# Performance work log

Hardware: AMD Instinct MI355X
Metric: run time of the kernel (lower is better)

The kernel has to match this reference:

```python
import jax, jax.numpy as jnp
import numpy as np

NUM_HEADS = 8
WS = 7          # window size (hardcoded in source)
SR = 4          # sr_ratio
EPS = 1e-5


def _win_partition(t, ws, H, W):
    # t: [B, h, N, d] -> [B*h*nW, ws*ws, d]
    B, h, N, d = t.shape
    t = t.reshape(B * h, H // ws, ws, W // ws, ws, d)
    t = t.transpose(0, 1, 3, 2, 4, 5)
    return t.reshape(-1, ws * ws, d)


def _win_reverse(w, ws, H, W, h):
    # w: [B*h*nW, ws*ws, d] -> [B, H*W, h*d]
    d = w.shape[-1]
    Bh = w.shape[0] // ((H // ws) * (W // ws))
    x = w.reshape(Bh, H // ws, W // ws, ws, ws, d).transpose(0, 1, 3, 2, 4, 5)
    x = x.reshape(Bh // h, h, H, W, d).transpose(0, 2, 3, 1, 4)
    return x.reshape(Bh // h, H * W, h * d)


def setup_inputs() -> dict:
    key = jax.random.key(0)
    B, H, W, C = 32, 56, 56, 256
    N = H * W
    ks = jax.random.split(key, 10)
    s = lambda k, shp: jax.random.normal(k, shp, dtype=jnp.float32) * 0.02
    return {
        "x": jax.random.normal(ks[0], (B, N, C), dtype=jnp.float32),
        "lepe_lin_w": s(ks[1], (C, C)), "lepe_lin_b": jnp.zeros((C,), jnp.float32),
        "lepe_conv_w": s(ks[2], (3, 3, 1, C)), "lepe_conv_b": jnp.zeros((C,), jnp.float32),
        "sr_w": s(ks[3], (SR, SR, C, C)), "sr_b": jnp.zeros((C,), jnp.float32),
        "norm_g": jnp.ones((C,), jnp.float32), "norm_b": jnp.zeros((C,), jnp.float32),
        "q1_w": s(ks[4], (C, C // 2)), "kv1_w": s(ks[5], (C, C)),
        "q2_w": s(ks[6], (C, C // 2)), "kv2_w": s(ks[7], (C, C)),
        "proj_w": s(ks[8], (C, C)), "proj_b": jnp.zeros((C,), jnp.float32),
        "H": H, "W": W,
    }


def reference(x, lepe_lin_w, lepe_lin_b, lepe_conv_w, lepe_conv_b, sr_w, sr_b,
              norm_g, norm_b, q1_w, kv1_w, q2_w, kv2_w, proj_w, proj_b, H, W):
    B, N, C = x.shape
    h2 = NUM_HEADS // 2
    d = C // NUM_HEADS
    scale = d ** (-0.5)

    # lepe: linear -> depthwise 3x3 conv (NHWC) -> flatten back
    lep = (x @ lepe_lin_w + lepe_lin_b).reshape(B, H, W, C)
    lep = jax.lax.conv_general_dilated(
        lep, lepe_conv_w, window_strides=(1, 1), padding='SAME',
        dimension_numbers=('NHWC', 'HWIO', 'NHWC'), feature_group_count=C) + lepe_conv_b
    lepe = lep.reshape(B, N, C)

    # --- branch 1: global attention over sr-downsampled kv ---
    q1 = (x @ q1_w).reshape(B, N, h2, d).transpose(0, 2, 1, 3)         # [B,h2,N,d]
    img = x.reshape(B, H, W, C)
    x1_ = jax.lax.conv_general_dilated(
        img, sr_w, window_strides=(SR, SR), padding='VALID',
        dimension_numbers=('NHWC', 'HWIO', 'NHWC')) + sr_b              # [B,H/sr,W/sr,C]
    x1_ = x1_.reshape(B, -1, C)                                         # [B,N1,C]
    mu = jnp.mean(x1_, axis=-1, keepdims=True)
    var = jnp.mean(jnp.square(x1_ - mu), axis=-1, keepdims=True)
    x1_ = (x1_ - mu) * jax.lax.rsqrt(var + EPS) * norm_g + norm_b
    x1_ = jax.nn.gelu(x1_, approximate=False)
    kv1 = (x1_ @ kv1_w).reshape(B, -1, 2, h2, d).transpose(2, 0, 3, 1, 4)
    k1, v1 = kv1[0], kv1[1]                                             # [B,h2,N1,d]
    attn1 = jax.nn.softmax(jnp.einsum('bhnd,bhmd->bhnm', q1, k1) * scale, axis=-1)
    x1 = jnp.einsum('bhnm,bhmd->bhnd', attn1, v1)
    x1 = x1.transpose(0, 2, 1, 3).reshape(B, N, C // 2)

    # --- branch 2: 7x7 window attention ---
    q2 = (x @ q2_w).reshape(B, N, h2, d).transpose(0, 2, 1, 3)          # [B,h2,N,d]
    kv2 = (x @ kv2_w).reshape(B, -1, 2, h2, d).transpose(2, 0, 3, 1, 4)
    k2, v2 = kv2[0], kv2[1]
    q2w = _win_partition(q2, WS, H, W)                                  # [B*h2*nW,49,d]
    k2w = _win_partition(k2, WS, H, W)
    v2w = _win_partition(v2, WS, H, W)
    attn2 = jax.nn.softmax(jnp.einsum('wnd,wmd->wnm', q2w, k2w) * scale, axis=-1)
    x2w = jnp.einsum('wnm,wmd->wnd', attn2, v2w)
    x2 = _win_reverse(x2w, WS, H, W, h2)                                # [B,N,C/2]

    out = jnp.concatenate([x1, x2], axis=-1)
    out = (out + lepe) @ proj_w + proj_b
    return out
```

## Files before the change

### kernel.cpp

```cpp
#include <hip/hip_runtime.h>
#include <hip/hip_bf16.h>

typedef __hip_bfloat16 bf16;
typedef __attribute__((ext_vector_type(8))) short short8;
typedef __attribute__((ext_vector_type(4))) float floatx4;

__device__ __forceinline__ float toF(bf16 v){ return __bfloat162float(v); }
__device__ __forceinline__ float b2f(unsigned short u){
  return __uint_as_float(((unsigned int)u) << 16);
}
__device__ __forceinline__ unsigned short f2bu(float f){
  bf16 h = __float2bfloat16(f);
  return *(unsigned short*)&h;
}

__device__ __forceinline__ void gl2l16(const void* g, void* l) {
  __builtin_amdgcn_global_load_lds(
      (const __attribute__((address_space(1))) unsigned int*)g,
      (__attribute__((address_space(3))) unsigned int*)l, 16, 0, 0);
}

__global__ __launch_bounds__(256) void cvt_x_kernel(
    const float* __restrict__ in, bf16* __restrict__ out) {
  size_t i4 = ((size_t)blockIdx.x * 256 + threadIdx.x) * 4;
  float4 v = *(const float4*)(in + i4);
  ushort4 o;
  o.x = f2bu(v.x); o.y = f2bu(v.y); o.z = f2bu(v.z); o.w = f2bu(v.w);
  *(ushort4*)(out + i4) = o;
}

__global__ __launch_bounds__(256) void prep_kernel(
    const float* __restrict__ sr_w, const float* __restrict__ lepe_w,
    const float* __restrict__ kv2_w, const float* __restrict__ q1_w,
    const float* __restrict__ q2_w, const float* __restrict__ kv1_w,
    const float* __restrict__ proj_w,
    bf16* __restrict__ wT_sr, bf16* __restrict__ wT_x,
    bf16* __restrict__ wT_kv1, bf16* __restrict__ wT_proj,
    int* __restrict__ srbase) {
  const int bid = blockIdx.x, tid = threadIdx.x;
  const float* src; bf16* dst; int K, N, idx;
  if (bid < 4096)      { src = sr_w;   dst = wT_sr;          K = 4096; N = 256; idx = bid * 256 + tid; }
  else if (bid < 4352) { src = lepe_w; dst = wT_x;           K = 256;  N = 256; idx = (bid - 4096) * 256 + tid; }
  else if (bid < 4608) { src = kv2_w;  dst = wT_x + 65536;   K = 256;  N = 256; idx = (bid - 4352) * 256 + tid; }
  else if (bid < 4736) { src = q1_w;   dst = wT_x + 131072;  K = 256;  N = 128; idx = (bid - 4608) * 256 + tid; }
  else if (bid < 4864) { src = q2_w;   dst = wT_x + 163840;  K = 256;  N = 128; idx = (bid - 4736) * 256 + tid; }
  else if (bid < 5120) { src = kv1_w;  dst = wT_kv1;         K = 256;  N = 256; idx = (bid - 4864) * 256 + tid; }
  else if (bid < 5376) { src = proj_w; dst = wT_proj;        K = 256;  N = 256; idx = (bid - 5120) * 256 + tid; }
  else {
    int t = (bid - 5376) * 256 + tid;
    if (t < 6272) {
      int b = t / 196, p = t - b * 196;
      int oy = p / 14, ox = p - oy * 14;
      srbase[t] = ((b * 56 + oy * 4) * 56 + ox * 4) * 256;
    }
    return;
  }
  int k = idx / N, n = idx - k * N;
  dst[(size_t)n * K + k] = __float2bfloat16(src[idx]);
}

__global__ __launch_bounds__(256) void gemm_mfma_f(
    const bf16* __restrict__ A, const bf16* __restrict__ BT,
    float* __restrict__ C, int K, int N) {
  __shared__ bf16 As[2][128 * 32];
  __shared__ bf16 Bs[2][128 * 32];
  const int tid = threadIdx.x;
  const int m0 = blockIdx.y * 128;
  const int n0 = blockIdx.x * 128;
  const int wave = tid >> 6, lane = tid & 63;
  const int wm = (wave >> 1) * 64, wn = (wave & 1) * 64;
  const int l15 = lane & 15, quad = lane >> 4;
  const int srow = lane >> 2, sseg = lane & 3;
  const bf16* aptr = A + (size_t)(m0 + wave * 32 + srow) * K + sseg * 8;
  const bf16* bptr = BT + (size_t)(n0 + wave * 32 + srow) * K + sseg * 8;
  const int rb = wave * 32;
  floatx4 zero = {0.f, 0.f, 0.f, 0.f};
  floatx4 acc[4][4];
#pragma unroll
  for (int i = 0; i < 4; i++)
#pragma unroll
    for (int j = 0; j < 4; j++) acc[i][j] = zero;

  const int NT = K >> 5;
  gl2l16(aptr, &As[0][rb * 32]);
  gl2l16(aptr + (size_t)16 * K, &As[0][(rb + 16) * 32]);
  gl2l16(bptr, &Bs[0][rb * 32]);
  gl2l16(bptr + (size_t)16 * K, &Bs[0][(rb + 16) * 32]);
  __syncthreads();
  int cur = 0;
  for (int t = 0; t < NT; t++) {
    if (t + 1 < NT) {
      int k0 = (t + 1) * 32;
      gl2l16(aptr + k0, &As[cur ^ 1][rb * 32]);
      gl2l16(aptr + (size_t)16 * K + k0, &As[cur ^ 1][(rb + 16) * 32]);
      gl2l16(bptr + k0, &Bs[cur ^ 1][rb * 32]);
      gl2l16(bptr + (size_t)16 * K + k0, &Bs[cur ^ 1][(rb + 16) * 32]);
    }
    short8 af[4], bfr[4];
#pragma unroll
    for (int i = 0; i < 4; i++)
      af[i] = *(const short8*)&As[cur][(wm + i * 16 + l15) * 32 + quad * 8];
#pragma unroll
    for (int j = 0; j < 4; j++)
      bfr[j] = *(const short8*)&Bs[cur][(wn + j * 16 + l15) * 32 + quad * 8];
#pragma unroll
    for (int i = 0; i < 4; i++)
#pragma unroll
      for (int j = 0; j < 4; j++)
        acc[i][j] = __builtin_amdgcn_mfma_f32_16x16x32_bf16(bfr[j], af[i], acc[i][j], 0, 0, 0);
    __syncthreads();
    cur ^= 1;
  }
#pragma unroll
  for (int i = 0; i < 4; i++) {
    int m = m0 + wm + i * 16 + l15;
#pragma unroll
    for (int j = 0; j < 4; j++) {
      int nb = n0 + wn + j * 16 + quad * 4;
      float4 o = {acc[i][j][0], acc[i][j][1], acc[i][j][2], acc[i][j][3]};
      *(float4*)&C[(size_t)m * N + nb] = o;
    }
  }
}

__global__ __launch_bounds__(256) void gemm_x3(
    const bf16* __restrict__ A, const bf16* __restrict__ BT,
    const float* __restrict__ lepe_b,
    bf16* __restrict__ L1, bf16* __restrict__ KV2, bf16* __restrict__ Q12) {
  __shared__ bf16 As[2][128 * 32];
  __shared__ bf16 Bs[2][128 * 32];
  const int sw = (blockIdx.x & 7) * 588 + (blockIdx.x >> 3);
  const int bx = sw % 6, by = sw / 6;
  const int m0 = by * 128;
  const int n0 = bx * 128;
  const int tid = threadIdx.x;
  const int wave = tid >> 6, lane = tid & 63;
  const int wm = (wave >> 1) * 64, wn = (wave & 1) * 64;
  const int l15 = lane & 15, quad = lane >> 4;
  const int srow = lane >> 2, sseg = lane & 3;
  const bf16* aptr = A + (size_t)(m0 + wave * 32 + srow) * 256 + sseg * 8;
  const bf16* bptr = BT + (size_t)(n0 + wave * 32 + srow) * 256 + sseg * 8;
  const int rb = wave * 32;
  floatx4 zero = {0.f, 0.f, 0.f, 0.f};
  floatx4 acc[4][4];
#pragma unroll
  for (int i = 0; i < 4; i++)
#pragma unroll
    for (int j = 0; j < 4; j++) acc[i][j] = zero;

  gl2l16(aptr, &As[0][rb * 32]);
  gl2l16(aptr + 16 * 256, &As[0][(rb + 16) * 32]);
  gl2l16(bptr, &Bs[0][rb * 32]);
  gl2l16(bptr + 16 * 256, &Bs[0][(rb + 16) * 32]);
  __syncthreads();
  int cur = 0;
#pragma unroll
  for (int t = 0; t < 8; t++) {
    if (t < 7) {
      int k0 = (t + 1) * 32;
      gl2l16(aptr + k0, &As[cur ^ 1][rb * 32]);
      gl2l16(aptr + 16 * 256 + k0, &As[cur ^ 1][(rb + 16) * 32]);
      gl2l16(bptr + k0, &Bs[cur ^ 1][rb * 32]);
      gl2l16(bptr + 16 * 256 + k0, &Bs[cur ^ 1][(rb + 16) * 32]);
    }
    short8 af[4], bfr[4];
#pragma unroll
    for (int i = 0; i < 4; i++)
      af[i] = *(const short8*)&As[cur][(wm + i * 16 + l15) * 32 + quad * 8];
#pragma unroll
    for (int j = 0; j < 4; j++)
      bfr[j] = *(const short8*)&Bs[cur][(wn + j * 16 + l15) * 32 + quad * 8];
#pragma unroll
    for (int i = 0; i < 4; i++)
#pragma unroll
      for (int j = 0; j < 4; j++)
        acc[i][j] = __builtin_amdgcn_mfma_f32_16x16x32_bf16(bfr[j], af[i], acc[i][j], 0, 0, 0);
    __syncthreads();
    cur ^= 1;
  }
  const int segN = n0 >> 8;
  bf16* Cd = (segN == 0) ? L1 : (segN == 1) ? KV2 : Q12;
  const int nc0 = n0 & 255;
#pragma unroll
  for (int i = 0; i < 4; i++) {
    int m = m0 + wm + i * 16 + l15;
#pragma unroll
    for (int j = 0; j < 4; j++) {
      int nb = nc0 + wn + j * 16 + quad * 4;
      float4 bv = {0.f, 0.f, 0.f, 0.f};
      if (segN == 0) bv = *(const float4*)&lepe_b[nb];
      ushort4 o;
      o.x = f2bu(acc[i][j][0] + bv.x);
      o.y = f2bu(acc[i][j][1] + bv.y);
      o.z = f2bu(acc[i][j][2] + bv.z);
      o.w = f2bu(acc[i][j][3] + bv.w);
      *(ushort4*)&Cd[(size_t)m * 256 + nb] = o;
    }
  }
}

__global__ __launch_bounds__(256) void gemm_sr(
    const bf16* __restrict__ X, const bf16* __restrict__ BT,
    const int* __restrict__ base, float* __restrict__ C) {
  __shared__ bf16 As[2][128 * 32];
  __shared__ bf16 Bs[2][128 * 32];
  const int tid = threadIdx.x;
  const int m0 = blockIdx.y * 128;
  const int n0 = blockIdx.x * 128;
  const int kz = blockIdx.z;
  const int wave = tid >> 6, lane = tid & 63;
  const int wm = (wave >> 1) * 64, wn = (wave & 1) * 64;
  const int l15 = lane & 15, quad = lane >> 4;
  const int srow = lane >> 2, sseg = lane & 3;
  const int mb0 = base[m0 + wave * 32 + srow];
  const int mb1 = base[m0 + wave * 32 + 16 + srow];
  const bf16* bptr = BT + (size_t)(n0 + wave * 32 + srow) * 4096 + sseg * 8;
  const int rb = wave * 32;
  const int kbeg = kz * 512;
  floatx4 zero = {0.f, 0.f, 0.f, 0.f};
  floatx4 acc[4][4];
#pragma unroll
  for (int i = 0; i < 4; i++)
#pragma unroll
    for (int j = 0; j < 4; j++) acc[i][j] = zero;

  {
    int k = kbeg + sseg * 8;
    int kp = k >> 8, c = k & 255;
    int off = ((kp >> 2) * 56 + (kp & 3)) * 256 + c;
    gl2l16(X + (size_t)mb0 + off, &As[0][rb * 32]);
    gl2l16(X + (size_t)mb1 + off, &As[0][(rb + 16) * 32]);
    gl2l16(bptr + kbeg, &Bs[0][rb * 32]);
    gl2l16(bptr + 16 * 4096 + kbeg, &Bs[0][(rb + 16) * 32]);
  }
  __syncthreads();
  int cur = 0;
  for (int t = 0; t < 16; t++) {
    if (t < 15) {
      int k = kbeg + (t + 1) * 32 + sseg * 8;
      int kp = k >> 8, c = k & 255;
      int off = ((kp >> 2) * 56 + (kp & 3)) * 256 + c;
      gl2l16(X + (size_t)mb0 + off, &As[cur ^ 1][rb * 32]);
      gl2l16(X + (size_t)mb1 + off, &As[cur ^ 1][(rb + 16) * 32]);
      gl2l16(bptr + kbeg + (t + 1) * 32, &Bs[cur ^ 1][rb * 32]);
      gl2l16(bptr + 16 * 4096 + kbeg + (t + 1) * 32, &Bs[cur ^ 1][(rb + 16) * 32]);
    }
    short8 af[4], bfr[4];
#pragma unroll
    for (int i = 0; i < 4; i++)
      af[i] = *(const short8*)&As[cur][(wm + i * 16 + l15) * 32 + quad * 8];
#pragma unroll
    for (int j = 0; j < 4; j++)
      bfr[j] = *(const short8*)&Bs[cur][(wn + j * 16 + l15) * 32 + quad * 8];
#pragma unroll
    for (int i = 0; i < 4; i++)
#pragma unroll
      for (int j = 0; j < 4; j++)
        acc[i][j] = __builtin_amdgcn_mfma_f32_16x16x32_bf16(bfr[j], af[i], acc[i][j], 0, 0, 0);
    __syncthreads();
    cur ^= 1;
  }
  float* Cp = C + (size_t)kz * (6272 * 256);
#pragma unroll
  for (int i = 0; i < 4; i++) {
    int m = m0 + wm + i * 16 + l15;
#pragma unroll
    for (int j = 0; j < 4; j++) {
      int nb = n0 + wn + j * 16 + quad * 4;
      float4 o = {acc[i][j][0], acc[i][j][1], acc[i][j][2], acc[i][j][3]};
      *(float4*)&Cp[(size_t)m * 256 + nb] = o;
    }
  }
}

__global__ __launch_bounds__(256) void gemm_proj_mfma(
    const bf16* __restrict__ X1, const bf16* __restrict__ X2,
    const bf16* __restrict__ L2, const bf16* __restrict__ BT,
    const float* __restrict__ bias, float* __restrict__ C) {
  __shared__ uint4 As[2][128 * 5];
  __shared__ bf16 Bs[2][128 * 32];
  const int sw = (blockIdx.x & 7) * 196 + (blockIdx.x >> 3);
  const int tid = threadIdx.x;
  const int m0 = (sw >> 1) * 128;
  const int n0 = (sw & 1) * 128;
  const int wave = tid >> 6, lane = tid & 63;
  const int wm = (wave >> 1) * 64, wn = (wave & 1) * 64;
  const int l15 = lane & 15, quad = lane >> 4;
  const int srow = lane >> 2, sseg = lane & 3;
  const bf16* bptr = BT + (size_t)(n0 + wave * 32 + srow) * 256 + sseg * 8;
  const int rb = wave * 32;
  const int row0 = tid >> 2, row1 = 64 + (tid >> 2), segA = tid & 3;
  floatx4 zero = {0.f, 0.f, 0.f, 0.f};
  floatx4 acc[4][4];
#pragma unroll
  for (int i = 0; i < 4; i++)
#pragma unroll
    for (int j = 0; j < 4; j++) acc[i][j] = zero;

  uint4 va0, va1, vl0, vl1;
  {
    int k = segA * 8;
    const bf16* s0 = (k < 128) ? X1 + (size_t)(m0 + row0) * 128 + k
                               : X2 + (size_t)(m0 + row0) * 128 + (k - 128);
    const bf16* s1 = (k < 128) ? X1 + (size_t)(m0 + row1) * 128 + k
                               : X2 + (size_t)(m0 + row1) * 128 + (k - 128);
    va0 = *(const uint4*)s0; va1 = *(const uint4*)s1;
    vl0 = *(const uint4*)(L2 + (size_t)(m0 + row0) * 256 + k);
    vl1 = *(const uint4*)(L2 + (size_t)(m0 + row1) * 256 + k);
  }
  gl2l16(bptr, &Bs[0][rb * 32]);
  gl2l16(bptr + 16 * 256, &Bs[0][(rb + 16) * 32]);
  {
    unsigned short o0[8], o1[8];
    const unsigned short* pa0 = (const unsigned short*)&va0;
    const unsigned short* pl0 = (const unsigned short*)&vl0;
    const unsigned short* pa1 = (const unsigned short*)&va1;
    const unsigned short* pl1 = (const unsigned short*)&vl1;
#pragma unroll
    for (int e = 0; e < 8; e++) {
      o0[e] = f2bu(b2f(pa0[e]) + b2f(pl0[e]));
      o1[e] = f2bu(b2f(pa1[e]) + b2f(pl1[e]));
    }
    As[0][row0 * 5 + segA] = *(const uint4*)o0;
    As[0][row1 * 5 + segA] = *(const uint4*)o1;
  }
  __syncthreads();
  int cur = 0;
#pragma unroll
  for (int t = 0; t < 8; t++) {
    uint4 nva0, nva1, nvl0, nvl1;
    if (t < 7) {
      int k0 = (t + 1) * 32;
      gl2l16(bptr + k0, &Bs[cur ^ 1][rb * 32]);
      gl2l16(bptr + 16 * 256 + k0, &Bs[cur ^ 1][(rb + 16) * 32]);
      int k = k0 + segA * 8;
      const bf16* s0 = (k < 128) ? X1 + (size_t)(m0 + row0) * 128 + k
                                 : X2 + (size_t)(m0 + row0) * 128 + (k - 128);
      const bf16* s1 = (k < 128) ? X1 + (size_t)(m0 + row1) * 128 + k
                                 : X2 + (size_t)(m0 + row1) * 128 + (k - 128);
      nva0 = *(const uint4*)s0; nva1 = *(const uint4*)s1;
      nvl0 = *(const uint4*)(L2 + (size_t)(m0 + row0) * 256 + k);
      nvl1 = *(const uint4*)(L2 + (size_t)(m0 + row1) * 256 + k);
    }
    short8 af[4], bfr[4];
#pragma unroll
    for (int i = 0; i < 4; i++)
      af[i] = *(const short8*)&As[cur][(wm + i * 16 + l15) * 5 + quad];
#pragma unroll
    for (int j = 0; j < 4; j++)
      bfr[j] = *(const short8*)&Bs[cur][(wn + j * 16 + l15) * 32 + quad * 8];
#pragma unroll
    for (int i = 0; i < 4; i++)
#pragma unroll
      for (int j = 0; j < 4; j++)
        acc[i][j] = __builtin_amdgcn_mfma_f32_16x16x32_bf16(bfr[j], af[i], acc[i][j], 0, 0, 0);
    if (t < 7) {
      unsigned short o0[8], o1[8];
      const unsigned short* pa0 = (const unsigned short*)&nva0;
      const unsigned short* pl0 = (const unsigned short*)&nvl0;
      const unsigned short* pa1 = (const unsigned short*)&nva1;
      const unsigned short* pl1 = (const unsigned short*)&nvl1;
#pragma unroll
      for (int e = 0; e < 8; e++) {
        o0[e] = f2bu(b2f(pa0[e]) + b2f(pl0[e]));
        o1[e] = f2bu(b2f(pa1[e]) + b2f(pl1[e]));
      }
      As[cur ^ 1][row0 * 5 + segA] = *(const uint4*)o0;
      As[cur ^ 1][row1 * 5 + segA] = *(const uint4*)o1;
    }
    __syncthreads();
    cur ^= 1;
  }
#pragma unroll
  for (int i = 0; i < 4; i++) {
    int m = m0 + wm + i * 16 + l15;
#pragma unroll
    for (int j = 0; j < 4; j++) {
      int nb = n0 + wn + j * 16 + quad * 4;
      float4 bv = *(const float4*)&bias[nb];
      float4 o = {acc[i][j][0] + bv.x, acc[i][j][1] + bv.y,
                  acc[i][j][2] + bv.z, acc[i][j][3] + bv.w};
      *(float4*)&C[(size_t)m * 256 + nb] = o;
    }
  }
}

__global__ __launch_bounds__(256) void dwconv8_kernel(
    const bf16* __restrict__ in, const float* __restrict__ w,
    const float* __restrict__ bias, bf16* __restrict__ out) {
  const int idx = blockIdx.x * 256 + threadIdx.x;
  const int c8 = (idx & 31) * 8;
  const int sp = idx >> 5;
  const int xx = sp % 56;
  const int yb = sp / 56;
  const int yy = yb % 56;
  const int b  = yb / 56;
  float4 bb0 = *(const float4*)&bias[c8];
  float4 bb1 = *(const float4*)&bias[c8 + 4];
  float acc[8] = {bb0.x, bb0.y, bb0.z, bb0.w, bb1.x, bb1.y, bb1.z, bb1.w};
#pragma unroll
  for (int dy = 0; dy < 3; dy++) {
    int y = yy + dy - 1;
    if ((unsigned)y >= 56u) continue;
#pragma unroll
    for (int dx = 0; dx < 3; dx++) {
      int x = xx + dx - 1;
      if ((unsigned)x >= 56u) continue;
      uint4 v = *(const uint4*)&in[((size_t)((b * 56 + y) * 56 + x)) * 256 + c8];
      const unsigned short* pv = (const unsigned short*)&v;
      float4 w0 = *(const float4*)&w[(dy * 3 + dx) * 256 + c8];
      float4 w1 = *(const float4*)&w[(dy * 3 + dx) * 256 + c8 + 4];
      float wf[8] = {w0.x, w0.y, w0.z, w0.w, w1.x, w1.y, w1.z, w1.w};
#pragma unroll
      for (int e = 0; e < 8; e++) acc[e] += b2f(pv[e]) * wf[e];
    }
  }
  unsigned short o[8];
#pragma unroll
  for (int e = 0; e < 8; e++) o[e] = f2bu(acc[e]);
  *(uint4*)&out[(size_t)sp * 256 + c8] = *(const uint4*)o;
}

__global__ __launch_bounds__(256) void ln_gelu_kernel(
    const float* __restrict__ in, const float* __restrict__ srb,
    const float* __restrict__ g, const float* __restrict__ bb,
    bf16* __restrict__ out) {
  const int tok = blockIdx.x;
  const int tid = threadIdx.x;
  float v = srb[tid];
  const float* p = in + (size_t)tok * 256 + tid;
#pragma unroll
  for (int c = 0; c < 8; c++) v += p[(size_t)c * 1605632];
  float s = v, s2 = v * v;
#pragma unroll
  for (int o = 32; o > 0; o >>= 1) {
    s += __shfl_down(s, o, 64);
    s2 += __shfl_down(s2, o, 64);
  }
  __shared__ float rs[4], rs2[4];
  int wid = tid >> 6, lane = tid & 63;
  if (lane == 0) { rs[wid] = s; rs2[wid] = s2; }
  __syncthreads();
  float tot = rs[0] + rs[1] + rs[2] + rs[3];
  float tot2 = rs2[0] + rs2[1] + rs2[2] + rs2[3];
  float mean = tot * (1.0f / 256.0f);
  float var = tot2 * (1.0f / 256.0f) - mean * mean;
  float y = (v - mean) * rsqrtf(var + 1e-5f) * g[tid] + bb[tid];
  out[(size_t)tok * 256 + tid] =
      __float2bfloat16(0.5f * y * (1.0f + erff(y * 0.70710678118654752f)));
}

__global__ __launch_bounds__(256) void attn1_mfma(
    const bf16* __restrict__ Q12, const float* __restrict__ KV,
    bf16* __restrict__ O) {
  __shared__ bf16 sk[224 * 32];
  __shared__ bf16 svT[32 * 232];
  __shared__ bf16 pbuf[4][64 * 32];
  const int b = blockIdx.z, h = blockIdx.y, chunk = blockIdx.x;
  const int tid = threadIdx.x;
  const int wave = tid >> 6, lane = tid & 63;
  const int l15 = lane & 15, quad = lane >> 4;
  for (int i = tid; i < 224 * 8; i += 256) {
    int m = i >> 3, c = i & 7;
    float4 kf = {0.f, 0.f, 0.f, 0.f}, vf = {0.f, 0.f, 0.f, 0.f};
    if (m < 196) {
      const float* p = KV + ((size_t)(b * 196 + m)) * 256 + h * 32 + c * 4;
      kf = *(const float4*)p;
      vf = *(const float4*)(p + 128);
    }
    ushort4 ko;
    ko.x = f2bu(kf.x); ko.y = f2bu(kf.y); ko.z = f2bu(kf.z); ko.w = f2bu(kf.w);
    *(ushort4*)&sk[m * 32 + c * 4] = ko;
    svT[(c * 4 + 0) * 232 + m] = __float2bfloat16(vf.x);
    svT[(c * 4 + 1) * 232 + m] = __float2bfloat16(vf.y);
    svT[(c * 4 + 2) * 232 + m] = __float2bfloat16(vf.z);
    svT[(c * 4 + 3) * 232 + m] = __float2bfloat16(vf.w);
  }
  __syncthreads();
  const int q0 = chunk * 256 + wave * 64;
  short8 aq[4];
#pragma unroll
  for (int i = 0; i < 4; i++) {
    int qr = q0 + i * 16 + l15; if (qr > 3135) qr = 3135;
    aq[i] = *(const short8*)(Q12 + ((size_t)(b * 3136 + qr)) * 256 + h * 32 + quad * 8);
  }
  const float scale = 0.17677669529663687f;
  floatx4 zero = {0.f, 0.f, 0.f, 0.f};
  floatx4 acc[4][2];
  float lsum[4][4];
#pragma unroll
  for (int i = 0; i < 4; i++) {
    acc[i][0] = zero; acc[i][1] = zero;
#pragma unroll
    for (int r = 0; r < 4; r++) lsum[i][r] = 0.f;
  }
  bf16* pw = pbuf[wave];
  for (int c = 0; c < 7; c++) {
    const int kv0 = c * 32;
    short8 bk[2];
#pragma unroll
    for (int n = 0; n < 2; n++)
      bk[n] = *(const short8*)&sk[(kv0 + n * 16 + l15) * 32 + quad * 8];
    floatx4 s[4][2];
#pragma unroll
    for (int i = 0; i < 4; i++)
#pragma unroll
      for (int n = 0; n < 2; n++)
        s[i][n] = __builtin_amdgcn_mfma_f32_16x16x32_bf16(aq[i], bk[n], zero, 0, 0, 0);
#pragma unroll
    for (int i = 0; i < 4; i++)
#pragma unroll
      for (int n = 0; n < 2; n++) {
        bool valid = (kv0 + n * 16 + l15) < 196;
#pragma unroll
        for (int r = 0; r < 4; r++) {
          float p = valid ? __expf(s[i][n][r] * scale) : 0.f;
          lsum[i][r] += p;
          pw[(i * 16 + quad * 4 + r) * 32 + n * 16 + l15] = __float2bfloat16(p);
        }
      }
    asm volatile("s_waitcnt lgkmcnt(0)" ::: "memory");
    short8 ap[4], bv[2];
#pragma unroll
    for (int i = 0; i < 4; i++)
      ap[i] = *(const short8*)&pw[(i * 16 + l15) * 32 + quad * 8];
#pragma unroll
    for (int n = 0; n < 2; n++)
      bv[n] = *(const short8*)&svT[(n * 16 + l15) * 232 + kv0 + quad * 8];
#pragma unroll
    for (int i = 0; i < 4; i++)
#pragma unroll
      for (int n = 0; n < 2; n++)
        acc[i][n] = __builtin_amdgcn_mfma_f32_16x16x32_bf16(ap[i], bv[n], acc[i][n], 0, 0, 0);
  }
#pragma unroll
  for (int i = 0; i < 4; i++)
#pragma unroll
    for (int r = 0; r < 4; r++) {
      float v = lsum[i][r];
      v += __shfl_xor(v, 1, 64);
      v += __shfl_xor(v, 2, 64);
      v += __shfl_xor(v, 4, 64);
      v += __shfl_xor(v, 8, 64);
      lsum[i][r] = 1.0f / v;
    }
#pragma unroll
  for (int i = 0; i < 4; i++)
#pragma unroll
    for (int r = 0; r < 4; r++) {
      int qr = q0 + i * 16 + quad * 4 + r;
      if (qr < 3136) {
        bf16* op = O + ((size_t)(b * 3136 + qr)) * 128 + h * 32;
        op[l15]      = __float2bfloat16(acc[i][0][r] * lsum[i][r]);
        op[16 + l15] = __float2bfloat16(acc[i][1][r] * lsum[i][r]);
      }
    }
}

__global__ __launch_bounds__(256) void attn2_mfma(
    const bf16* __restrict__ Q12, const bf16* __restrict__ KV2,
    bf16* __restrict__ O) {
  __shared__ bf16 sk[64 * 136];
  __shared__ bf16 pb[4][64 * 72];
  const int b = blockIdx.y;
  const int win = blockIdx.x;
  const int wy = win >> 3, wx = win & 7;
  const int tid = threadIdx.x;
  const int wave = tid >> 6, lane = tid & 63;
  const int l15 = lane & 15, quad = lane >> 4;
  const int h = wave;

  for (int i = tid; i < 49 * 16; i += 256) {
    int m = i >> 4, c = i & 15;
    int iy = m / 7, ix = m - iy * 7;
    int n = (wy * 7 + iy) * 56 + wx * 7 + ix;
    *(uint4*)&sk[m * 136 + c * 8] =
        *(const uint4*)&KV2[((size_t)(b * 3136 + n)) * 256 + c * 8];
  }

  short8 bvv[2][2];
#pragma unroll
  for (int ks = 0; ks < 2; ks++)
#pragma unroll
    for (int nt = 0; nt < 2; nt++)
#pragma unroll
      for (int e = 0; e < 8; e++) {
        int k = ks * 32 + quad * 8 + e; if (k > 48) k = 48;
        int iy = k / 7, ix = k - iy * 7;
        int n = (wy * 7 + iy) * 56 + wx * 7 + ix;
        bvv[ks][nt][e] = ((const short*)KV2)[((size_t)(b * 3136 + n)) * 256
                                             + 128 + h * 32 + nt * 16 + l15];
      }

  short8 aq[4];
#pragma unroll
  for (int i = 0; i < 4; i++) {
    int lq = i * 16 + l15; if (lq > 48) lq = 48;
    int iy = lq / 7, ix = lq - iy * 7;
    int n = (wy * 7 + iy) * 56 + wx * 7 + ix;
    aq[i] = *(const short8*)(Q12 + ((size_t)(b * 3136 + n)) * 256 + 128 + h * 32 + quad * 8);
  }
  __syncthreads();

  const float scale = 0.17677669529663687f;
  floatx4 zero = {0.f, 0.f, 0.f, 0.f};
  floatx4 acc[4][2];
  float lsum[4][4];
#pragma unroll
  for (int i = 0; i < 4; i++) {
    acc[i][0] = zero; acc[i][1] = zero;
#pragma unroll
    for (int r = 0; r < 4; r++) lsum[i][r] = 0.f;
  }
  bf16* pw = pb[wave];
#pragma unroll
  for (int c = 0; c < 2; c++) {
    const int kv0 = c * 32;
    short8 bk[2];
#pragma unroll
    for (int n = 0; n < 2; n++)
      bk[n] = *(const short8*)&sk[(kv0 + n * 16 + l15) * 136 + h * 32 + quad * 8];
    floatx4 s[4][2];
#pragma unroll
    for (int i = 0; i < 4; i++)
#pragma unroll
      for (int n = 0; n < 2; n++)
        s[i][n] = __builtin_amdgcn_mfma_f32_16x16x32_bf16(aq[i], bk[n], zero, 0, 0, 0);
#pragma unroll
    for (int i = 0; i < 4; i++)
#pragma unroll
      for (int n = 0; n < 2; n++) {
        bool valid = (kv0 + n * 16 + l15) < 49;
#pragma unroll
        for (int r = 0; r < 4; r++) {
          float p = valid ? __expf(s[i][n][r] * scale) : 0.f;
          lsum[i][r] += p;
          pw[(i * 16 + quad * 4 + r) * 72 + kv0 + n * 16 + l15] = __float2bfloat16(p);
        }
      }
  }
  asm volatile("s_waitcnt lgkmcnt(0)" ::: "memory");
#pragma unroll
  for (int ks = 0; ks < 2; ks++) {
    short8 ap[4];
#pragma unroll
    for (int i = 0; i < 4; i++)
      ap[i] = *(const short8*)&pw[(i * 16 + l15) * 72 + ks * 32 + quad * 8];
#pragma unroll
    for (int i = 0; i < 4; i++)
#pragma unroll
      for (int nt = 0; nt < 2; nt++)
        acc[i][nt] = __builtin_amdgcn_mfma_f32_16x16x32_bf16(ap[i], bvv[ks][nt], acc[i][nt], 0, 0, 0);
  }
#pragma unroll
  for (int i = 0; i < 4; i++)
#pragma unroll
    for (int r = 0; r < 4; r++) {
      float v = lsum[i][r];
      v += __shfl_xor(v, 1, 64);
      v += __shfl_xor(v, 2, 64);
      v += __shfl_xor(v, 4, 64);
      v += __shfl_xor(v, 8, 64);
      lsum[i][r] = 1.0f / v;
    }
#pragma unroll
  for (int i = 0; i < 4; i++)
#pragma unroll
    for (int r = 0; r < 4; r++) {
      int lq = i * 16 + quad * 4 + r;
      if (lq < 49) {
        int iy = lq / 7, ix = lq - iy * 7;
        int n = (wy * 7 + iy) * 56 + wx * 7 + ix;
        bf16* op = O + ((size_t)(b * 3136 + n)) * 128 + h * 32;
        op[l15]      = __float2bfloat16(acc[i][0][r] * lsum[i][r]);
        op[16 + l15] = __float2bfloat16(acc[i][1][r] * lsum[i][r]);
      }
    }
}

extern "C" void kernel_launch(void* const* d_in, const int* in_sizes, int n_in,
                              void* d_out, int out_size, void* d_ws, size_t ws_size,
                              hipStream_t stream) {
  const float* x           = (const float*)d_in[0];
  const float* lepe_lin_w  = (const float*)d_in[1];
  const float* lepe_lin_b  = (const float*)d_in[2];
  const float* lepe_conv_w = (const float*)d_in[3];
  const float* lepe_conv_b = (const float*)d_in[4];
  const float* sr_w        = (const float*)d_in[5];
  const float* sr_b        = (const float*)d_in[6];
  const float* norm_g      = (const float*)d_in[7];
  const float* norm_b      = (const float*)d_in[8];
  const float* q1_w        = (const float*)d_in[9];
  const float* kv1_w       = (const float*)d_in[10];
  const float* q2_w        = (const float*)d_in[11];
  const float* kv2_w       = (const float*)d_in[12];
  const float* proj_w      = (const float*)d_in[13];
  const float* proj_b      = (const float*)d_in[14];
  float* out = (float*)d_out;

  char* ws = (char*)d_ws;
  char* ob = (char*)d_out;
  const size_t szBNC = 100352ull * 256 * 2;
  const size_t szBNh = 100352ull * 128 * 2;
  bf16*  xb  = (bf16*)ob;
  bf16*  Q12 = (bf16*)(ob + szBNC);
  bf16*  L1  = (bf16*)ws;
  float* X1Ppart = (float*)ws;
  bf16*  X1N = (bf16*)ob;
  float* KV1 = (float*)(ob + 8388608);
  bf16*  X1  = (bf16*)ws;
  bf16*  L2  = (bf16*)(ws + szBNC);
  bf16*  X2  = (bf16*)(ws + 2 * szBNC);
  char*  wtb = ws + 2 * szBNC + szBNh;
  bf16* wT_x    = (bf16*)(wtb);
  bf16* wT_kv1  = (bf16*)(wtb + 393216);
  bf16* wT_proj = (bf16*)(wtb + 524288);
  bf16* wT_sr   = (bf16*)(wtb + 655360);
  int*  srbase  = (int*)(wtb + 655360 + 2097152);
  bf16* KV2     = (bf16*)(wtb + 655360 + 2097152 + 32768);

  cvt_x_kernel<<<25088, 256, 0, stream>>>(x, xb);
  prep_kernel<<<5401, 256, 0, stream>>>(
      sr_w, lepe_lin_w, kv2_w, q1_w, q2_w, kv1_w, proj_w,
      wT_sr, wT_x, wT_kv1, wT_proj, srbase);

  gemm_x3<<<4704, 256, 0, stream>>>(xb, wT_x, lepe_lin_b, L1, KV2, Q12);

  dwconv8_kernel<<<12544, 256, 0, stream>>>(L1, lepe_conv_w, lepe_conv_b, L2);

  attn2_mfma<<<dim3(64, 32), 256, 0, stream>>>(Q12, KV2, X2);

  gemm_sr<<<dim3(2, 49, 8), 256, 0, stream>>>(xb, wT_sr, srbase, X1Ppart);
  ln_gelu_kernel<<<6272, 256, 0, stream>>>(X1Ppart, sr_b, norm_g, norm_b, X1N);
  gemm_mfma_f<<<dim3(2, 49), 256, 0, stream>>>(X1N, wT_kv1, KV1, 256, 256);
  attn1_mfma<<<dim3(13, 4, 32), 256, 0, stream>>>(Q12, KV1, X1);

  gemm_proj_mfma<<<1568, 256, 0, stream>>>(
      X1, X2, L2, wT_proj, proj_b, out);
}
```

Baseline: 536.5 us.

## Replace LDS-direct loads with register-staged padded tiles, fuse prep kernels, bf16 KV1

Every MFMA GEMM now loads global tiles into registers and stores them to a single padded LDS buffer (stride 5 uint4) instead of double-buffered global_load_lds. This aims to remove LDS bank conflicts and reduce LDS footprint for higher occupancy, at the cost of a synchronization per tile without a double buffer. The x conversion and weight-prep kernels are merged into one launch. The kv1 GEMM now writes bf16 instead of fp32, and attn1 reads bf16 directly, which halves that traffic and drops the in-kernel conversion.

```diff
diff --git a/kernel.cpp b/kernel.cpp
--- a/kernel.cpp
+++ b/kernel.cpp
@@ -14,22 +14,8 @@
   return *(unsigned short*)&h;
 }
 
-__device__ __forceinline__ void gl2l16(const void* g, void* l) {
-  __builtin_amdgcn_global_load_lds(
-      (const __attribute__((address_space(1))) unsigned int*)g,
-      (__attribute__((address_space(3))) unsigned int*)l, 16, 0, 0);
-}
-
-__global__ __launch_bounds__(256) void cvt_x_kernel(
-    const float* __restrict__ in, bf16* __restrict__ out) {
-  size_t i4 = ((size_t)blockIdx.x * 256 + threadIdx.x) * 4;
-  float4 v = *(const float4*)(in + i4);
-  ushort4 o;
-  o.x = f2bu(v.x); o.y = f2bu(v.y); o.z = f2bu(v.z); o.w = f2bu(v.w);
-  *(ushort4*)(out + i4) = o;
-}
-
-__global__ __launch_bounds__(256) void prep_kernel(
+__global__ __launch_bounds__(256) void prep_all_kernel(
+    const float* __restrict__ x, bf16* __restrict__ xb,
     const float* __restrict__ sr_w, const float* __restrict__ lepe_w,
     const float* __restrict__ kv2_w, const float* __restrict__ q1_w,
     const float* __restrict__ q2_w, const float* __restrict__ kv1_w,
@@ -37,7 +23,16 @@
     bf16* __restrict__ wT_sr, bf16* __restrict__ wT_x,
     bf16* __restrict__ wT_kv1, bf16* __restrict__ wT_proj,
     int* __restrict__ srbase) {
-  const int bid = blockIdx.x, tid = threadIdx.x;
+  const int tid = threadIdx.x;
+  if (blockIdx.x < 25088) {
+    size_t i4 = ((size_t)blockIdx.x * 256 + tid) * 4;
+    float4 v = *(const float4*)(x + i4);
+    ushort4 o;
+    o.x = f2bu(v.x); o.y = f2bu(v.y); o.z = f2bu(v.z); o.w = f2bu(v.w);
+    *(ushort4*)(xb + i4) = o;
+    return;
+  }
+  const int bid = blockIdx.x - 25088;
   const float* src; bf16* dst; int K, N, idx;
   if (bid < 4096)      { src = sr_w;   dst = wT_sr;          K = 4096; N = 256; idx = bid * 256 + tid; }
   else if (bid < 4352) { src = lepe_w; dst = wT_x;           K = 256;  N = 256; idx = (bid - 4096) * 256 + tid; }
@@ -59,76 +54,12 @@
   dst[(size_t)n * K + k] = __float2bfloat16(src[idx]);
 }
 
-__global__ __launch_bounds__(256) void gemm_mfma_f(
-    const bf16* __restrict__ A, const bf16* __restrict__ BT,
-    float* __restrict__ C, int K, int N) {
-  __shared__ bf16 As[2][128 * 32];
-  __shared__ bf16 Bs[2][128 * 32];
-  const int tid = threadIdx.x;
-  const int m0 = blockIdx.y * 128;
-  const int n0 = blockIdx.x * 128;
-  const int wave = tid >> 6, lane = tid & 63;
-  const int wm = (wave >> 1) * 64, wn = (wave & 1) * 64;
-  const int l15 = lane & 15, quad = lane >> 4;
-  const int srow = lane >> 2, sseg = lane & 3;
-  const bf16* aptr = A + (size_t)(m0 + wave * 32 + srow) * K + sseg * 8;
-  const bf16* bptr = BT + (size_t)(n0 + wave * 32 + srow) * K + sseg * 8;
-  const int rb = wave * 32;
-  floatx4 zero = {0.f, 0.f, 0.f, 0.f};
-  floatx4 acc[4][4];
-#pragma unroll
-  for (int i = 0; i < 4; i++)
-#pragma unroll
-    for (int j = 0; j < 4; j++) acc[i][j] = zero;
-
-  const int NT = K >> 5;
-  gl2l16(aptr, &As[0][rb * 32]);
-  gl2l16(aptr + (size_t)16 * K, &As[0][(rb + 16) * 32]);
-  gl2l16(bptr, &Bs[0][rb * 32]);
-  gl2l16(bptr + (size_t)16 * K, &Bs[0][(rb + 16) * 32]);
-  __syncthreads();
-  int cur = 0;
-  for (int t = 0; t < NT; t++) {
-    if (t + 1 < NT) {
-      int k0 = (t + 1) * 32;
-      gl2l16(aptr + k0, &As[cur ^ 1][rb * 32]);
-      gl2l16(aptr + (size_t)16 * K + k0, &As[cur ^ 1][(rb + 16) * 32]);
-      gl2l16(bptr + k0, &Bs[cur ^ 1][rb * 32]);
-      gl2l16(bptr + (size_t)16 * K + k0, &Bs[cur ^ 1][(rb + 16) * 32]);
-    }
-    short8 af[4], bfr[4];
-#pragma unroll
-    for (int i = 0; i < 4; i++)
-      af[i] = *(const short8*)&As[cur][(wm + i * 16 + l15) * 32 + quad * 8];
-#pragma unroll
-    for (int j = 0; j < 4; j++)
-      bfr[j] = *(const short8*)&Bs[cur][(wn + j * 16 + l15) * 32 + quad * 8];
-#pragma unroll
-    for (int i = 0; i < 4; i++)
-#pragma unroll
-      for (int j = 0; j < 4; j++)
-        acc[i][j] = __builtin_amdgcn_mfma_f32_16x16x32_bf16(bfr[j], af[i], acc[i][j], 0, 0, 0);
-    __syncthreads();
-    cur ^= 1;
-  }
-#pragma unroll
-  for (int i = 0; i < 4; i++) {
-    int m = m0 + wm + i * 16 + l15;
-#pragma unroll
-    for (int j = 0; j < 4; j++) {
-      int nb = n0 + wn + j * 16 + quad * 4;
-      float4 o = {acc[i][j][0], acc[i][j][1], acc[i][j][2], acc[i][j][3]};
-      *(float4*)&C[(size_t)m * N + nb] = o;
-    }
-  }
-}
-
 __global__ __launch_bounds__(256) void gemm_x3(
     const bf16* __restrict__ A, const bf16* __restrict__ BT,
     const float* __restrict__ lepe_b,
     bf16* __restrict__ L1, bf16* __restrict__ KV2, bf16* __restrict__ Q12) {
-  __shared__ bf16 As[2][128 * 32];
-  __shared__ bf16 Bs[2][128 * 32];
+  __shared__ uint4 As[128 * 5];
+  __shared__ uint4 Bs[128 * 5];
   const int sw = (blockIdx.x & 7) * 588 + (blockIdx.x >> 3);
   const int bx = sw % 6, by = sw / 6;
   const int m0 = by * 128;
@@ -137,10 +68,11 @@
   const int wave = tid >> 6, lane = tid & 63;
   const int wm = (wave >> 1) * 64, wn = (wave & 1) * 64;
   const int l15 = lane & 15, quad = lane >> 4;
-  const int srow = lane >> 2, sseg = lane & 3;
-  const bf16* aptr = A + (size_t)(m0 + wave * 32 + srow) * 256 + sseg * 8;
-  const bf16* bptr = BT + (size_t)(n0 + wave * 32 + srow) * 256 + sseg * 8;
-  const int rb = wave * 32;
+  const int row0 = tid >> 2, row1 = 64 + (tid >> 2), seg = tid & 3;
+  const bf16* aP0 = A + (size_t)(m0 + row0) * 256 + seg * 8;
+  const bf16* aP1 = A + (size_t)(m0 + row1) * 256 + seg * 8;
+  const bf16* bP0 = BT + (size_t)(n0 + row0) * 256 + seg * 8;
+  const bf16* bP1 = BT + (size_t)(n0 + row1) * 256 + seg * 8;
   floatx4 zero = {0.f, 0.f, 0.f, 0.f};
   floatx4 acc[4][4];
 #pragma unroll
@@ -148,35 +80,31 @@
 #pragma unroll
     for (int j = 0; j < 4; j++) acc[i][j] = zero;
 
-  gl2l16(aptr, &As[0][rb * 32]);
-  gl2l16(aptr + 16 * 256, &As[0][(rb + 16) * 32]);
-  gl2l16(bptr, &Bs[0][rb * 32]);
-  gl2l16(bptr + 16 * 256, &Bs[0][(rb + 16) * 32]);
-  __syncthreads();
-  int cur = 0;
+  uint4 a0 = *(const uint4*)aP0, a1 = *(const uint4*)aP1;
+  uint4 b0 = *(const uint4*)bP0, b1 = *(const uint4*)bP1;
 #pragma unroll
   for (int t = 0; t < 8; t++) {
+    As[row0 * 5 + seg] = a0; As[row1 * 5 + seg] = a1;
+    Bs[row0 * 5 + seg] = b0; Bs[row1 * 5 + seg] = b1;
+    __syncthreads();
     if (t < 7) {
       int k0 = (t + 1) * 32;
-      gl2l16(aptr + k0, &As[cur ^ 1][rb * 32]);
-      gl2l16(aptr + 16 * 256 + k0, &As[cur ^ 1][(rb + 16) * 32]);
-      gl2l16(bptr + k0, &Bs[cur ^ 1][rb * 32]);
-      gl2l16(bptr + 16 * 256 + k0, &Bs[cur ^ 1][(rb + 16) * 32]);
+      a0 = *(const uint4*)(aP0 + k0); a1 = *(const uint4*)(aP1 + k0);
+      b0 = *(const uint4*)(bP0 + k0); b1 = *(const uint4*)(bP1 + k0);
     }
     short8 af[4], bfr[4];
 #pragma unroll
     for (int i = 0; i < 4; i++)
-      af[i] = *(const short8*)&As[cur][(wm + i * 16 + l15) * 32 + quad * 8];
+      af[i] = *(const short8*)&As[(wm + i * 16 + l15) * 5 + quad];
 #pragma unroll
     for (int j = 0; j < 4; j++)
-      bfr[j] = *(const short8*)&Bs[cur][(wn + j * 16 + l15) * 32 + quad * 8];
+      bfr[j] = *(const short8*)&Bs[(wn + j * 16 + l15) * 5 + quad];
 #pragma unroll
     for (int i = 0; i < 4; i++)
 #pragma unroll
       for (int j = 0; j < 4; j++)
         acc[i][j] = __builtin_amdgcn_mfma_f32_16x16x32_bf16(bfr[j], af[i], acc[i][j], 0, 0, 0);
     __syncthreads();
-    cur ^= 1;
   }
   const int segN = n0 >> 8;
   bf16* Cd = (segN == 0) ? L1 : (segN == 1) ? KV2 : Q12;
@@ -202,8 +130,8 @@
 __global__ __launch_bounds__(256) void gemm_sr(
     const bf16* __restrict__ X, const bf16* __restrict__ BT,
     const int* __restrict__ base, float* __restrict__ C) {
-  __shared__ bf16 As[2][128 * 32];
-  __shared__ bf16 Bs[2][128 * 32];
+  __shared__ uint4 As[128 * 5];
+  __shared__ uint4 Bs[128 * 5];
   const int tid = threadIdx.x;
   const int m0 = blockIdx.y * 128;
   const int n0 = blockIdx.x * 128;
@@ -211,11 +139,11 @@
   const int wave = tid >> 6, lane = tid & 63;
   const int wm = (wave >> 1) * 64, wn = (wave & 1) * 64;
   const int l15 = lane & 15, quad = lane >> 4;
-  const int srow = lane >> 2, sseg = lane & 3;
-  const int mb0 = base[m0 + wave * 32 + srow];
-  const int mb1 = base[m0 + wave * 32 + 16 + srow];
-  const bf16* bptr = BT + (size_t)(n0 + wave * 32 + srow) * 4096 + sseg * 8;
-  const int rb = wave * 32;
+  const int row0 = tid >> 2, row1 = 64 + (tid >> 2), seg = tid & 3;
+  const int mb0 = base[m0 + row0];
+  const int mb1 = base[m0 + row1];
+  const bf16* bP0 = BT + (size_t)(n0 + row0) * 4096 + seg * 8;
+  const bf16* bP1 = BT + (size_t)(n0 + row1) * 4096 + seg * 8;
   const int kbeg = kz * 512;
   floatx4 zero = {0.f, 0.f, 0.f, 0.f};
   floatx4 acc[4][4];
@@ -224,41 +152,42 @@
 #pragma unroll
     for (int j = 0; j < 4; j++) acc[i][j] = zero;
 
+  uint4 a0, a1, b0, b1;
   {
-    int k = kbeg + sseg * 8;
+    int k = kbeg + seg * 8;
     int kp = k >> 8, c = k & 255;
     int off = ((kp >> 2) * 56 + (kp & 3)) * 256 + c;
-    gl2l16(X + (size_t)mb0 + off, &As[0][rb * 32]);
-    gl2l16(X + (size_t)mb1 + off, &As[0][(rb + 16) * 32]);
-    gl2l16(bptr + kbeg, &Bs[0][rb * 32]);
-    gl2l16(bptr + 16 * 4096 + kbeg, &Bs[0][(rb + 16) * 32]);
-  }
-  __syncthreads();
-  int cur = 0;
+    a0 = *(const uint4*)(X + (size_t)mb0 + off);
+    a1 = *(const uint4*)(X + (size_t)mb1 + off);
+    b0 = *(const uint4*)(bP0 + kbeg);
+    b1 = *(const uint4*)(bP1 + kbeg);
+  }
   for (int t = 0; t < 16; t++) {
+    As[row0 * 5 + seg] = a0; As[row1 * 5 + seg] = a1;
+    Bs[row0 * 5 + seg] = b0; Bs[row1 * 5 + seg] = b1;
+    __syncthreads();
     if (t < 15) {
-      int k = kbeg + (t + 1) * 32 + sseg * 8;
+      int k = kbeg + (t + 1) * 32 + seg * 8;
       int kp = k >> 8, c = k & 255;
       int off = ((kp >> 2) * 56 + (kp & 3)) * 256 + c;
-      gl2l16(X + (size_t)mb0 + off, &As[cur ^ 1][rb * 32]);
-      gl2l16(X + (size_t)mb1 + off, &As[cur ^ 1][(rb + 16) * 32]);
-      gl2l16(bptr + kbeg + (t + 1) * 32, &Bs[cur ^ 1][rb * 32]);
-      gl2l16(bptr + 16 * 4096 + kbeg + (t + 1) * 32, &Bs[cur ^ 1][(rb + 16) * 32]);
+      a0 = *(const uint4*)(X + (size_t)mb0 + off);
+      a1 = *(const uint4*)(X + (size_t)mb1 + off);
+      b0 = *(const uint4*)(bP0 + kbeg + (t + 1) * 32);
+      b1 = *(const uint4*)(bP1 + kbeg + (t + 1) * 32);
     }
     short8 af[4], bfr[4];
 #pragma unroll
     for (int i = 0; i < 4; i++)
-      af[i] = *(const short8*)&As[cur][(wm + i * 16 + l15) * 32 + quad * 8];
+      af[i] = *(const short8*)&As[(wm + i * 16 + l15) * 5 + quad];
 #pragma unroll
     for (int j = 0; j < 4; j++)
-      bfr[j] = *(const short8*)&Bs[cur][(wn + j * 16 + l15) * 32 + quad * 8];
+      bfr[j] = *(const short8*)&Bs[(wn + j * 16 + l15) * 5 + quad];
 #pragma unroll
     for (int i = 0; i < 4; i++)
 #pragma unroll
       for (int j = 0; j < 4; j++)
         acc[i][j] = __builtin_amdgcn_mfma_f32_16x16x32_bf16(bfr[j], af[i], acc[i][j], 0, 0, 0);
     __syncthreads();
-    cur ^= 1;
   }
   float* Cp = C + (size_t)kz * (6272 * 256);
 #pragma unroll
@@ -273,12 +202,75 @@
   }
 }
 
+__global__ __launch_bounds__(256) void gemm_kv1(
+    const bf16* __restrict__ A, const bf16* __restrict__ BT,
+    bf16* __restrict__ C) {
+  __shared__ uint4 As[128 * 5];
+  __shared__ uint4 Bs[128 * 5];
+  const int tid = threadIdx.x;
+  const int m0 = blockIdx.y * 128;
+  const int n0 = blockIdx.x * 128;
+  const int wave = tid >> 6, lane = tid & 63;
+  const int wm = (wave >> 1) * 64, wn = (wave & 1) * 64;
+  const int l15 = lane & 15, quad = lane >> 4;
+  const int row0 = tid >> 2, row1 = 64 + (tid >> 2), seg = tid & 3;
+  const bf16* aP0 = A + (size_t)(m0 + row0) * 256 + seg * 8;
+  const bf16* aP1 = A + (size_t)(m0 + row1) * 256 + seg * 8;
+  const bf16* bP0 = BT + (size_t)(n0 + row0) * 256 + seg * 8;
+  const bf16* bP1 = BT + (size_t)(n0 + row1) * 256 + seg * 8;
+  floatx4 zero = {0.f, 0.f, 0.f, 0.f};
+  floatx4 acc[4][4];
+#pragma unroll
+  for (int i = 0; i < 4; i++)
+#pragma unroll
+    for (int j = 0; j < 4; j++) acc[i][j] = zero;
+
+  uint4 a0 = *(const uint4*)aP0, a1 = *(const uint4*)aP1;
+  uint4 b0 = *(const uint4*)bP0, b1 = *(const uint4*)bP1;
+#pragma unroll
+  for (int t = 0; t < 8; t++) {
+    As[row0 * 5 + seg] = a0; As[row1 * 5 + seg] = a1;
+    Bs[row0 * 5 + seg] = b0; Bs[row1 * 5 + seg] = b1;
+    __syncthreads();
+    if (t < 7) {
+      int k0 = (t + 1) * 32;
+      a0 = *(const uint4*)(aP0 + k0); a1 = *(const uint4*)(aP1 + k0);
+      b0 = *(const uint4*)(bP0 + k0); b1 = *(const uint4*)(bP1 + k0);
+    }
+    short8 af[4], bfr[4];
+#pragma unroll
+    for (int i = 0; i < 4; i++)
+      af[i] = *(const short8*)&As[(wm + i * 16 + l15) * 5 + quad];
+#pragma unroll
+    for (int j = 0; j < 4; j++)
+      bfr[j] = *(const short8*)&Bs[(wn + j * 16 + l15) * 5 + quad];
+#pragma unroll
+    for (int i = 0; i < 4; i++)
+#pragma unroll
+      for (int j = 0; j < 4; j++)
+        acc[i][j] = __builtin_amdgcn_mfma_f32_16x16x32_bf16(bfr[j], af[i], acc[i][j], 0, 0, 0);
+    __syncthreads();
+  }
+#pragma unroll
+  for (int i = 0; i < 4; i++) {
+    int m = m0 + wm + i * 16 + l15;
+#pragma unroll
+    for (int j = 0; j < 4; j++) {
+      int nb = n0 + wn + j * 16 + quad * 4;
+      ushort4 o;
+      o.x = f2bu(acc[i][j][0]); o.y = f2bu(acc[i][j][1]);
+      o.z = f2bu(acc[i][j][2]); o.w = f2bu(acc[i][j][3]);
+      *(ushort4*)&C[(size_t)m * 256 + nb] = o;
+    }
+  }
+}
+
 __global__ __launch_bounds__(256) void gemm_proj_mfma(
     const bf16* __restrict__ X1, const bf16* __restrict__ X2,
     const bf16* __restrict__ L2, const bf16* __restrict__ BT,
     const float* __restrict__ bias, float* __restrict__ C) {
-  __shared__ uint4 As[2][128 * 5];
-  __shared__ bf16 Bs[2][128 * 32];
+  __shared__ uint4 As[128 * 5];
+  __shared__ uint4 Bs[128 * 5];
   const int sw = (blockIdx.x & 7) * 196 + (blockIdx.x >> 3);
   const int tid = threadIdx.x;
   const int m0 = (sw >> 1) * 128;
@@ -286,10 +278,9 @@
   const int wave = tid >> 6, lane = tid & 63;
   const int wm = (wave >> 1) * 64, wn = (wave & 1) * 64;
   const int l15 = lane & 15, quad = lane >> 4;
-  const int srow = lane >> 2, sseg = lane & 3;
-  const bf16* bptr = BT + (size_t)(n0 + wave * 32 + srow) * 256 + sseg * 8;
-  const int rb = wave * 32;
-  const int row0 = tid >> 2, row1 = 64 + (tid >> 2), segA = tid & 3;
+  const int row0 = tid >> 2, row1 = 64 + (tid >> 2), seg = tid & 3;
+  const bf16* bP0 = BT + (size_t)(n0 + row0) * 256 + seg * 8;
+  const bf16* bP1 = BT + (size_t)(n0 + row1) * 256 + seg * 8;
   floatx4 zero = {0.f, 0.f, 0.f, 0.f};
   floatx4 acc[4][4];
 #pragma unroll
@@ -297,79 +288,60 @@
 #pragma unroll
     for (int j = 0; j < 4; j++) acc[i][j] = zero;
 
-  uint4 va0, va1, vl0, vl1;
+  uint4 va0, va1, vl0, vl1, b0, b1;
   {
-    int k = segA * 8;
-    const bf16* s0 = (k < 128) ? X1 + (size_t)(m0 + row0) * 128 + k
-                               : X2 + (size_t)(m0 + row0) * 128 + (k - 128);
-    const bf16* s1 = (k < 128) ? X1 + (size_t)(m0 + row1) * 128 + k
-                               : X2 + (size_t)(m0 + row1) * 128 + (k - 128);
+    int k = seg * 8;
+    const bf16* s0 = X1 + (size_t)(m0 + row0) * 128 + k;
+    const bf16* s1 = X1 + (size_t)(m0 + row1) * 128 + k;
     va0 = *(const uint4*)s0; va1 = *(const uint4*)s1;
     vl0 = *(const uint4*)(L2 + (size_t)(m0 + row0) * 256 + k);
     vl1 = *(const uint4*)(L2 + (size_t)(m0 + row1) * 256 + k);
-  }
-  gl2l16(bptr, &Bs[0][rb * 32]);
-  gl2l16(bptr + 16 * 256, &Bs[0][(rb + 16) * 32]);
-  {
-    unsigned short o0[8], o1[8];
-    const unsigned short* pa0 = (const unsigned short*)&va0;
-    const unsigned short* pl0 = (const unsigned short*)&vl0;
-    const unsigned short* pa1 = (const unsigned short*)&va1;
-    const unsigned short* pl1 = (const unsigned short*)&vl1;
-#pragma unroll
-    for (int e = 0; e < 8; e++) {
-      o0[e] = f2bu(b2f(pa0[e]) + b2f(pl0[e]));
-      o1[e] = f2bu(b2f(pa1[e]) + b2f(pl1[e]));
-    }
-    As[0][row0 * 5 + segA] = *(const uint4*)o0;
-    As[0][row1 * 5 + segA] = *(const uint4*)o1;
-  }
-  __syncthreads();
-  int cur = 0;
+    b0 = *(const uint4*)bP0; b1 = *(const uint4*)bP1;
+  }
 #pragma unroll
   for (int t = 0; t < 8; t++) {
-    uint4 nva0, nva1, nvl0, nvl1;
+    {
+      unsigned short o0[8], o1[8];
+      const unsigned short* pa0 = (const unsigned short*)&va0;
+      const unsigned short* pl0 = (const unsigned short*)&vl0;
+      const unsigned short* pa1 = (const unsigned short*)&va1;
+      const unsigned short* pl1 = (const unsigned short*)&vl1;
+#pragma unroll
+      for (int e = 0; e < 8; e++) {
+        o0[e] = f2bu(b2f(pa0[e]) + b2f(pl0[e]));
+        o1[e] = f2bu(b2f(pa1[e]) + b2f(pl1[e]));
+      }
+      As[row0 * 5 + seg] = *(const uint4*)o0;
+      As[row1 * 5 + seg] = *(const uint4*)o1;
+      Bs[row0 * 5 + seg] = b0;
+      Bs[row1 * 5 + seg] = b1;
+    }
+    __syncthreads();
     if (t < 7) {
-      int k0 = (t + 1) * 32;
-      gl2l16(bptr + k0, &Bs[cur ^ 1][rb * 32]);
-      gl2l16(bptr + 16 * 256 + k0, &Bs[cur ^ 1][(rb + 16) * 32]);
-      int k = k0 + segA * 8;
+      int k = (t + 1) * 32 + seg * 8;
       const bf16* s0 = (k < 128) ? X1 + (size_t)(m0 + row0) * 128 + k
                                  : X2 + (size_t)(m0 + row0) * 128 + (k - 128);
       const bf16* s1 = (k < 128) ? X1 + (size_t)(m0 + row1) * 128 + k
                                  : X2 + (size_t)(m0 + row1) * 128 + (k - 128);
-      nva0 = *(const uint4*)s0; nva1 = *(const uint4*)s1;
-      nvl0 = *(const uint4*)(L2 + (size_t)(m0 + row0) * 256 + k);
-      nvl1 = *(const uint4*)(L2 + (size_t)(m0 + row1) * 256 + k);
+      va0 = *(const uint4*)s0; va1 = *(const uint4*)s1;
+      vl0 = *(const uint4*)(L2 + (size_t)(m0 + row0) * 256 + k);
+      vl1 = *(const uint4*)(L2 + (size_t)(m0 + row1) * 256 + k);
+      b0 = *(const uint4*)(bP0 + (t + 1) * 32);
+      b1 = *(const uint4*)(bP1 + (t + 1) * 32);
     }
     short8 af[4], bfr[4];
 #pragma unroll
     for (int i = 0; i < 4; i++)
-      af[i] = *(const short8*)&As[cur][(wm + i * 16 + l15) * 5 + quad];
+      af[i] = *(const short8*)&As[(wm + i * 16 + l15) * 5 + quad];
 #pragma unroll
     for (int j = 0; j < 4; j++)
-      bfr[j] = *(const short8*)&Bs[cur][(wn + j * 16 + l15) * 32 + quad * 8];
+      bfr[j] = *(const short8*)&Bs[(wn + j * 16 + l15) * 5 + quad];
 #pragma unroll
     for (int i = 0; i < 4; i++)
 #pragma unroll
       for (int j = 0; j < 4; j++)
         acc[i][j] = __builtin_amdgcn_mfma_f32_16x16x32_bf16(bfr[j], af[i], acc[i][j], 0, 0, 0);
-    if (t < 7) {
-      unsigned short o0[8], o1[8];
-      const unsigned short* pa0 = (const unsigned short*)&nva0;
-      const unsigned short* pl0 = (const unsigned short*)&nvl0;
-      const unsigned short* pa1 = (const unsigned short*)&nva1;
-      const unsigned short* pl1 = (const unsigned short*)&nvl1;
-#pragma unroll
-      for (int e = 0; e < 8; e++) {
-        o0[e] = f2bu(b2f(pa0[e]) + b2f(pl0[e]));
-        o1[e] = f2bu(b2f(pa1[e]) + b2f(pl1[e]));
-      }
-      As[cur ^ 1][row0 * 5 + segA] = *(const uint4*)o0;
-      As[cur ^ 1][row1 * 5 + segA] = *(const uint4*)o1;
-    }
     __syncthreads();
-    cur ^= 1;
   }
 #pragma unroll
   for (int i = 0; i < 4; i++) {
@@ -451,7 +423,7 @@
 }
 
 __global__ __launch_bounds__(256) void attn1_mfma(
-    const bf16* __restrict__ Q12, const float* __restrict__ KV,
+    const bf16* __restrict__ Q12, const bf16* __restrict__ KV,
     bf16* __restrict__ O) {
   __shared__ bf16 sk[224 * 32];
   __shared__ bf16 svT[32 * 232];
@@ -460,21 +432,19 @@
   const int tid = threadIdx.x;
   const int wave = tid >> 6, lane = tid & 63;
   const int l15 = lane & 15, quad = lane >> 4;
-  for (int i = tid; i < 224 * 8; i += 256) {
-    int m = i >> 3, c = i & 7;
-    float4 kf = {0.f, 0.f, 0.f, 0.f}, vf = {0.f, 0.f, 0.f, 0.f};
+  for (int i = tid; i < 224 * 4; i += 256) {
+    int m = i >> 2, c = i & 3;
+    uint4 kv4 = {0u, 0u, 0u, 0u}, vv4 = {0u, 0u, 0u, 0u};
     if (m < 196) {
-      const float* p = KV + ((size_t)(b * 196 + m)) * 256 + h * 32 + c * 4;
-      kf = *(const float4*)p;
-      vf = *(const float4*)(p + 128);
-    }
-    ushort4 ko;
-    ko.x = f2bu(kf.x); ko.y = f2bu(kf.y); ko.z = f2bu(kf.z); ko.w = f2bu(kf.w);
-    *(ushort4*)&sk[m * 32 + c * 4] = ko;
-    svT[(c * 4 + 0) * 232 + m] = __float2bfloat16(vf.x);
-    svT[(c * 4 + 1) * 232 + m] = __float2bfloat16(vf.y);
-    svT[(c * 4 + 2) * 232 + m] = __float2bfloat16(vf.z);
-    svT[(c * 4 + 3) * 232 + m] = __float2bfloat16(vf.w);
+      const bf16* p = KV + ((size_t)(b * 196 + m)) * 256 + h * 32 + c * 8;
+      kv4 = *(const uint4*)p;
+      vv4 = *(const uint4*)(p + 128);
+    }
+    *(uint4*)&sk[m * 32 + c * 8] = kv4;
+    const unsigned short* pv = (const unsigned short*)&vv4;
+#pragma unroll
+    for (int e = 0; e < 8; e++)
+      *(unsigned short*)&svT[(c * 8 + e) * 232 + m] = pv[e];
   }
   __syncthreads();
   const int q0 = chunk * 256 + wave * 64;
@@ -707,7 +677,7 @@
   bf16*  L1  = (bf16*)ws;
   float* X1Ppart = (float*)ws;
   bf16*  X1N = (bf16*)ob;
-  float* KV1 = (float*)(ob + 8388608);
+  bf16*  KV1 = (bf16*)(ob + 8388608);
   bf16*  X1  = (bf16*)ws;
   bf16*  L2  = (bf16*)(ws + szBNC);
   bf16*  X2  = (bf16*)(ws + 2 * szBNC);
@@ -719,9 +689,8 @@
   int*  srbase  = (int*)(wtb + 655360 + 2097152);
   bf16* KV2     = (bf16*)(wtb + 655360 + 2097152 + 32768);
 
-  cvt_x_kernel<<<25088, 256, 0, stream>>>(x, xb);
-  prep_kernel<<<5401, 256, 0, stream>>>(
-      sr_w, lepe_lin_w, kv2_w, q1_w, q2_w, kv1_w, proj_w,
+  prep_all_kernel<<<30489, 256, 0, stream>>>(
+      x, xb, sr_w, lepe_lin_w, kv2_w, q1_w, q2_w, kv1_w, proj_w,
       wT_sr, wT_x, wT_kv1, wT_proj, srbase);
 
   gemm_x3<<<4704, 256, 0, stream>>>(xb, wT_x, lepe_lin_b, L1, KV2, Q12);
@@ -732,7 +701,7 @@
 
   gemm_sr<<<dim3(2, 49, 8), 256, 0, stream>>>(xb, wT_sr, srbase, X1Ppart);
   ln_gelu_kernel<<<6272, 256, 0, stream>>>(X1Ppart, sr_b, norm_g, norm_b, X1N);
-  gemm_mfma_f<<<dim3(2, 49), 256, 0, stream>>>(X1N, wT_kv1, KV1, 256, 256);
+  gemm_kv1<<<dim3(2, 49), 256, 0, stream>>>(X1N, wT_kv1, KV1);
   attn1_mfma<<<dim3(13, 4, 32), 256, 0, stream>>>(Q12, KV1, X1);
 
   gemm_proj_mfma<<<1568, 256, 0, stream>>>(
```

Result: no change. 527.8 us (-1.6%).
